# Performance work log

Measured on AMD Instinct MI355X. Metric: run time of the kernel, lower is better.

Reference implementation:

```python
import math
import jax, jax.numpy as jnp
import numpy as np

H = 1024
NH = 16
HD = H // NH
FF = 4096


def gelu_erf(x):
    return x * 0.5 * (1.0 + jax.lax.erf(x / jnp.sqrt(jnp.float32(2.0))))


def layernorm(x, gamma, beta, eps=1e-12):
    mean = x.mean(axis=-1, keepdims=True)
    var = ((x - mean) ** 2).mean(axis=-1, keepdims=True)
    return gamma * (x - mean) / jnp.sqrt(var + eps) + beta


def setup_inputs() -> dict:
    key = jax.random.key(0)
    ks = jax.random.split(key, 12)
    B, S = 2, 2048
    sc = 0.02
    return {
        "x": jax.random.normal(ks[0], (B, S, H), jnp.float32),
        "attention_mask": jnp.ones((B, S), jnp.int32),
        "Wq": jax.random.normal(ks[1], (H, H), jnp.float32) * sc,
        "bq": jnp.zeros((H,), jnp.float32),
        "Wk": jax.random.normal(ks[2], (H, H), jnp.float32) * sc,
        "bk": jnp.zeros((H,), jnp.float32),
        "Wv": jax.random.normal(ks[3], (H, H), jnp.float32) * sc,
        "bv": jnp.zeros((H,), jnp.float32),
        "Wo": jax.random.normal(ks[4], (H, H), jnp.float32) * sc,
        "bo": jnp.zeros((H,), jnp.float32),
        "ln1_g": jnp.ones((H,), jnp.float32),
        "ln1_b": jnp.zeros((H,), jnp.float32),
        "W1": jax.random.normal(ks[5], (H, FF), jnp.float32) * sc,
        "b1": jnp.zeros((FF,), jnp.float32),
        "W2": jax.random.normal(ks[6], (FF, H), jnp.float32) * sc,
        "b2": jnp.zeros((H,), jnp.float32),
        "ln2_g": jnp.ones((H,), jnp.float32),
        "ln2_b": jnp.zeros((H,), jnp.float32),
    }


def reference(x, attention_mask, Wq, bq, Wk, bk, Wv, bv, Wo, bo,
              ln1_g, ln1_b, W1, b1, W2, b2, ln2_g, ln2_b):
    B, S, _ = x.shape
    # QKV projections, split heads -> [B, NH, S, HD]
    def split(t):
        return t.reshape(B, S, NH, HD).transpose(0, 2, 1, 3)
    q = split(x @ Wq + bq)
    k = split(x @ Wk + bk)
    v = split(x @ Wv + bv)
    # scores [B, NH, S, S]
    s = jnp.einsum("bhqd,bhkd->bhqk", q, k) / math.sqrt(HD)
    mask = (attention_mask == 1)[:, None, None, :]  # [B,1,1,S]
    s = jnp.where(mask, s, -jnp.inf)
    p = jax.nn.softmax(s, axis=-1)
    a = jnp.einsum("bhqk,bhkd->bhqd", p, v)
    a = a.transpose(0, 2, 1, 3).reshape(B, S, H)  # merge heads
    a = a @ Wo + bo
    a = layernorm(a, ln1_g, ln1_b)  # NOTE: no residual in source
    m = gelu_erf(a @ W1 + b1) @ W2 + b2
    return layernorm(m, ln2_g, ln2_b)
```

## Files before the change

kernel.cpp:

```cpp
#include <hip/hip_runtime.h>
#include <hip/hip_bf16.h>
#include <math.h>

typedef __bf16 bf16;
typedef __attribute__((ext_vector_type(8))) __bf16 bf16x8;
typedef __attribute__((ext_vector_type(4))) __bf16 bf16x4;
typedef __attribute__((ext_vector_type(4))) float f32x4;
typedef __attribute__((ext_vector_type(4))) short short4v;

#define HDIM 1024
#define NHEAD 16
#define HD 64
#define FFDIM 4096
#define BATCH 2
#define SEQ 2048
#define M_TOK 4096
#define NSPLIT 2
#define PSTRIDE ((size_t)M_TOK * HDIM)

static __device__ __forceinline__ void async_load16(const bf16* g, bf16* l) {
  __builtin_amdgcn_global_load_lds(
      (const __attribute__((address_space(1))) void*)g,
      (__attribute__((address_space(3))) void*)l, 16, 0, 0);
}

static __device__ __forceinline__ f32x4 mfma16_bf16(bf16x4 a, bf16x4 b, f32x4 c) {
#if defined(__HIP_DEVICE_COMPILE__)
#if __has_builtin(__builtin_amdgcn_mfma_f32_16x16x16bf16_1k)
  return __builtin_amdgcn_mfma_f32_16x16x16bf16_1k(
      __builtin_bit_cast(short4v, a), __builtin_bit_cast(short4v, b), c, 0, 0, 0);
#else
  return __builtin_amdgcn_mfma_f32_16x16x16_bf16(a, b, c, 0, 0, 0);
#endif
#else
  return c;
#endif
}

__global__ __launch_bounds__(256)
void prep_kernel(const float* __restrict__ x,
                 const float* __restrict__ Wq, const float* __restrict__ Wk,
                 const float* __restrict__ Wv, const float* __restrict__ Wo,
                 const float* __restrict__ W1, const float* __restrict__ W2,
                 bf16* __restrict__ Xb, bf16* __restrict__ QKVT,
                 bf16* __restrict__ W1T, bf16* __restrict__ W2T)
{
  const int z = blockIdx.z;
  const int t = threadIdx.x;
  if (z == 12) {
    const size_t base = ((size_t)(blockIdx.y * 32 + blockIdx.x)) * 4096;
#pragma unroll
    for (int j = 0; j < 4; ++j) {
      const size_t i = base + j * 1024 + t * 4;
      f32x4 v = *(const f32x4*)(x + i);
      bf16x4 o;
#pragma unroll
      for (int k = 0; k < 4; ++k) o[k] = (bf16)v[k];
      *(bf16x4*)(Xb + i) = o;
    }
    return;
  }
  const float* ps; bf16* pd; int sld, dld;
  if (z < 4) {
    ps = (z == 0) ? Wq : (z == 1) ? Wk : (z == 2) ? Wv : Wo;
    pd = QKVT + (size_t)z * HDIM * HDIM; sld = 1024; dld = 1024;
  } else if (z < 8) {
    const int c = z - 4;
    ps = W1 + c * 1024; sld = 4096;
    pd = W1T + (size_t)c * 1024 * 1024; dld = 1024;
  } else {
    const int c = z - 8;
    ps = W2 + (size_t)c * 1024 * 1024; sld = 1024;
    pd = W2T + c * 1024; dld = 4096;
  }
  __shared__ float tile[32][33];
  const int tx = t & 31, ty = t >> 5;
  const int c0 = blockIdx.x * 32, r0 = blockIdx.y * 32;
#pragma unroll
  for (int i = 0; i < 32; i += 8)
    tile[ty + i][tx] = ps[(size_t)(r0 + ty + i) * sld + c0 + tx];
  __syncthreads();
#pragma unroll
  for (int i = 0; i < 32; i += 8)
    pd[(size_t)(c0 + ty + i) * dld + r0 + tx] = (bf16)tile[tx][ty + i];
}

template<int EPI>
__global__ __launch_bounds__(256)
void gemm_bt(const bf16* __restrict__ A, const bf16* __restrict__ Bt,
             const float* __restrict__ b0, const float* __restrict__ b1p,
             const float* __restrict__ b2p, void* __restrict__ Cout,
             int M, int N, int ldk, int kchunk)
{
  __shared__ __align__(16) bf16 As[128 * 64];
  __shared__ __align__(16) bf16 Bs[128 * 64];
  const int t = threadIdx.x;
  const int wave = t >> 6, lane = t & 63;
  const int lm = lane & 15, qd = lane >> 4;
  const int wm = (wave >> 1) * 64, wn = (wave & 1) * 64;
  const int bm = blockIdx.y * 128, bn = blockIdx.x * 128;
  const int kbeg = blockIdx.z * kchunk;

  f32x4 acc[4][4] = {};
  const int srow = t >> 3;
  const int schk = t & 7;

  for (int k0 = kbeg; k0 < kbeg + kchunk; k0 += 64) {
#pragma unroll
    for (int r = 0; r < 4; ++r) {
      const int row = r * 32 + srow;
      const int chunk = schk ^ (row & 7);
      async_load16(A + (size_t)(bm + row) * ldk + (k0 + chunk * 8),
                   (bf16*)((char*)As + r * 4096 + t * 16));
    }
#pragma unroll
    for (int r = 0; r < 4; ++r) {
      const int row = r * 32 + srow;
      const int chunk = schk ^ (row & 7);
      async_load16(Bt + (size_t)(bn + row) * ldk + (k0 + chunk * 8),
                   (bf16*)((char*)Bs + r * 4096 + t * 16));
    }
    __syncthreads();
#pragma unroll
    for (int ks = 0; ks < 2; ++ks) {
      bf16x8 av[4], bv[4];
#pragma unroll
      for (int mt = 0; mt < 4; ++mt) {
        const int row = wm + mt * 16 + lm;
        const int chunk = (ks * 4 + qd) ^ (row & 7);
        av[mt] = *(const bf16x8*)(As + row * 64 + chunk * 8);
      }
#pragma unroll
      for (int nt = 0; nt < 4; ++nt) {
        const int row = wn + nt * 16 + lm;
        const int chunk = (ks * 4 + qd) ^ (row & 7);
        bv[nt] = *(const bf16x8*)(Bs + row * 64 + chunk * 8);
      }
#pragma unroll
      for (int mt = 0; mt < 4; ++mt)
#pragma unroll
        for (int nt = 0; nt < 4; ++nt)
          acc[mt][nt] = __builtin_amdgcn_mfma_f32_16x16x32_bf16(bv[nt], av[mt], acc[mt][nt], 0, 0, 0);
    }
    __syncthreads();
  }

#pragma unroll
  for (int nt = 0; nt < 4; ++nt) {
    const int n0 = bn + wn + nt * 16 + qd * 4;
    f32x4 bsv = {0.f, 0.f, 0.f, 0.f};
    if (EPI == 2) bsv = *(const f32x4*)(b0 + n0);
    if (EPI == 3) {
      const int sect = n0 >> 10, c = n0 & 1023;
      const float* bp = (sect == 0) ? b0 : (sect == 1) ? b1p : b2p;
      bsv = *(const f32x4*)(bp + c);
    }
#pragma unroll
    for (int mt = 0; mt < 4; ++mt) {
      const int m = bm + wm + mt * 16 + lm;
      f32x4 v;
#pragma unroll
      for (int r = 0; r < 4; ++r) v[r] = acc[mt][nt][r] + bsv[r];
      if (EPI == 1) {
        *(f32x4*)((float*)Cout + (size_t)blockIdx.z * M * N + (size_t)m * N + n0) = v;
      } else if (EPI == 2) {
        bf16x4 o;
#pragma unroll
        for (int r = 0; r < 4; ++r) {
          const float z = v[r] * 0.70710678118f;
          const float az = fabsf(z);
          const float tt = __builtin_amdgcn_rcpf(fmaf(az, 0.3275911f, 1.0f));
          const float poly = tt * fmaf(tt, fmaf(tt, fmaf(tt, fmaf(tt, 1.061405429f,
                             -1.453152027f), 1.421413741f), -0.284496736f), 0.254829592f);
          const float e = __builtin_amdgcn_exp2f(az * az * -1.4426950408889634f);
          float erfv = 1.0f - poly * e;
          erfv = (z < 0.f) ? -erfv : erfv;
          o[r] = (bf16)(0.5f * v[r] * (1.0f + erfv));
        }
        *(bf16x4*)((bf16*)Cout + (size_t)m * N + n0) = o;
      } else {
        bf16* base = (bf16*)Cout;
        const int sect = n0 >> 10, c = n0 & 1023;
        if (sect < 2) {
          bf16x4 o;
#pragma unroll
          for (int r = 0; r < 4; ++r) o[r] = (bf16)v[r];
          *(bf16x4*)(base + (size_t)sect * M_TOK * HDIM + (size_t)m * HDIM + c) = o;
        } else {
          const int hh = c >> 6, dd = c & 63;
          const int bb = m >> 11, ss = m & 2047;
#pragma unroll
          for (int r = 0; r < 4; ++r)
            base[(size_t)2 * M_TOK * HDIM +
                 (size_t)((bb * NHEAD + hh) * HD + dd + r) * SEQ + ss] = (bf16)v[r];
        }
      }
    }
  }
}

__global__ __launch_bounds__(256)
void attn_kernel(const bf16* __restrict__ Q, const bf16* __restrict__ Kg,
                 const bf16* __restrict__ Vt, const int* __restrict__ mask,
                 float* __restrict__ Po, float* __restrict__ Lp)
{
  __shared__ __align__(16) bf16 Ks[64 * 64];
  __shared__ __align__(16) bf16 Vs[64 * 64];
  __shared__ float madd[64];

  const int t = threadIdx.x;
  const int wave = t >> 6, lane = t & 63;
  const int lm = lane & 15, qd = lane >> 4;
  const int bh = blockIdx.y;
  const int b = bh >> 4, h = bh & 15;
  const int q0 = blockIdx.x * 64;
  const int qg = q0 + wave * 16 + lm;
  const int split = blockIdx.z;
  const int kv_beg = split * (SEQ / NSPLIT);

  bf16x8 qf[2];
#pragma unroll
  for (int ks = 0; ks < 2; ++ks)
    qf[ks] = *(const bf16x8*)(Q + (size_t)(b * SEQ + qg) * HDIM + h * HD + ks * 32 + qd * 8);

  float l_lane = 0.f;
  f32x4 oacc[4] = {};

  const int srow = t >> 3, schk = t & 7;
  const float C = 0.1803368801f;

  for (int kv0 = kv_beg; kv0 < kv_beg + SEQ / NSPLIT; kv0 += 64) {
#pragma unroll
    for (int r = 0; r < 2; ++r) {
      const int row = r * 32 + srow;
      const int g = schk ^ (row & 7);
      async_load16(Kg + (size_t)(b * SEQ + kv0 + row) * HDIM + h * HD + g * 8,
                   (bf16*)((char*)Ks + r * 4096 + t * 16));
      async_load16(Vt + (size_t)(bh * HD + row) * SEQ + kv0 + g * 8,
                   (bf16*)((char*)Vs + r * 4096 + t * 16));
    }
    if (t < 64) madd[t] = (mask[b * SEQ + kv0 + t] == 1) ? 0.f : -1.0e30f;
    __syncthreads();

    f32x4 sacc[4] = {};
#pragma unroll
    for (int ks = 0; ks < 2; ++ks) {
#pragma unroll
      for (int nt = 0; nt < 4; ++nt) {
        const int row = nt * 16 + lm;
        const int c = (ks * 4 + qd) ^ (row & 7);
        bf16x8 kf = *(const bf16x8*)(Ks + row * 64 + c * 8);
        sacc[nt] = __builtin_amdgcn_mfma_f32_16x16x32_bf16(kf, qf[ks], sacc[nt], 0, 0, 0);
      }
    }

    bf16x4 pf4[4];
#pragma unroll
    for (int nt = 0; nt < 4; ++nt) {
      f32x4 ma = *(const f32x4*)(madd + nt * 16 + qd * 4);
#pragma unroll
      for (int r = 0; r < 4; ++r) {
        const float pv = __builtin_amdgcn_exp2f(fmaf(sacc[nt][r], C, ma[r]));
        l_lane += pv;
        pf4[nt][r] = (bf16)pv;
      }
    }

#pragma unroll
    for (int nt2 = 0; nt2 < 4; ++nt2) {
      const int row = nt2 * 16 + lm;
#pragma unroll
      for (int nt = 0; nt < 4; ++nt) {
        bf16x4 vf = *(const bf16x4*)(Vs + row * 64 +
                     (((nt * 2 + (qd >> 1)) ^ (row & 7)) * 8) + (qd & 1) * 4);
        oacc[nt2] = mfma16_bf16(vf, pf4[nt], oacc[nt2]);
      }
    }
    __syncthreads();
  }

  float l = l_lane;
  l += __shfl_xor(l, 16, 64);
  l += __shfl_xor(l, 32, 64);

  float* po = Po + ((size_t)(split * 32 + bh) * 64) * SEQ;
#pragma unroll
  for (int nt2 = 0; nt2 < 4; ++nt2)
#pragma unroll
    for (int r = 0; r < 4; ++r)
      po[(size_t)(nt2 * 16 + qd * 4 + r) * SEQ + q0 + wave * 16 + lm] = oacc[nt2][r];
  if (qd == 0)
    Lp[(size_t)(split * 32 + bh) * SEQ + q0 + wave * 16 + lm] = l;
}

__global__ __launch_bounds__(256)
void attn_merge(const float* __restrict__ Po, const float* __restrict__ Lp,
                bf16* __restrict__ Aout)
{
  const int t = threadIdx.x;
  const int bh = blockIdx.y;
  const int b = bh >> 4, h = bh & 15;
  const int s0 = blockIdx.x * 64;
  const int tok = t >> 2;
  const int dc = (t & 3) * 16;

  const float l = Lp[(size_t)bh * SEQ + s0 + tok] +
                  Lp[(size_t)(32 + bh) * SEQ + s0 + tok];
  const float inv = 1.0f / l;

  const float* p0 = Po + ((size_t)bh * 64) * SEQ + s0 + tok;
  const float* p1 = Po + ((size_t)(32 + bh) * 64) * SEQ + s0 + tok;
  bf16x8 o0, o1;
#pragma unroll
  for (int j = 0; j < 8; ++j)
    o0[j] = (bf16)((p0[(size_t)(dc + j) * SEQ] + p1[(size_t)(dc + j) * SEQ]) * inv);
#pragma unroll
  for (int j = 8; j < 16; ++j)
    o1[j - 8] = (bf16)((p0[(size_t)(dc + j) * SEQ] + p1[(size_t)(dc + j) * SEQ]) * inv);

  bf16* dst = Aout + (size_t)(b * SEQ + s0 + tok) * HDIM + h * HD + dc;
  *(bf16x8*)dst = o0;
  *(bf16x8*)(dst + 8) = o1;
}

template<int NP, int OUT_BF16>
__global__ __launch_bounds__(256)
void ln_sum(const float* __restrict__ p, const float* __restrict__ bias,
            const float* __restrict__ gamma, const float* __restrict__ beta,
            void* __restrict__ out)
{
  const int row = blockIdx.x;
  const int t = threadIdx.x;
  f32x4 v = *(const f32x4*)(p + (size_t)row * HDIM + t * 4);
#pragma unroll
  for (int np = 1; np < NP; ++np) {
    f32x4 u = *(const f32x4*)(p + np * PSTRIDE + (size_t)row * HDIM + t * 4);
#pragma unroll
    for (int j = 0; j < 4; ++j) v[j] += u[j];
  }
  f32x4 bv0 = *(const f32x4*)(bias + t * 4);
#pragma unroll
  for (int j = 0; j < 4; ++j) v[j] += bv0[j];

  float s = v[0] + v[1] + v[2] + v[3];
  float s2 = v[0] * v[0] + v[1] * v[1] + v[2] * v[2] + v[3] * v[3];
#pragma unroll
  for (int d = 1; d < 64; d <<= 1) { s += __shfl_xor(s, d, 64); s2 += __shfl_xor(s2, d, 64); }
  __shared__ float ss[4], ss2[4];
  const int wave = t >> 6, lane = t & 63;
  if (lane == 0) { ss[wave] = s; ss2[wave] = s2; }
  __syncthreads();
  s = ss[0] + ss[1] + ss[2] + ss[3];
  s2 = ss2[0] + ss2[1] + ss2[2] + ss2[3];
  const float mean = s * (1.0f / HDIM);
  const float var = s2 * (1.0f / HDIM) - mean * mean;
  const float rstd = rsqrtf(var + 1e-12f);
  f32x4 gv = *(const f32x4*)(gamma + t * 4);
  f32x4 bv = *(const f32x4*)(beta + t * 4);
  f32x4 y;
#pragma unroll
  for (int j = 0; j < 4; ++j) y[j] = gv[j] * (v[j] - mean) * rstd + bv[j];
  if (OUT_BF16) {
    bf16x4 o;
#pragma unroll
    for (int j = 0; j < 4; ++j) o[j] = (bf16)y[j];
    *(bf16x4*)((bf16*)out + (size_t)row * HDIM + t * 4) = o;
  } else {
    *(f32x4*)((float*)out + (size_t)row * HDIM + t * 4) = y;
  }
}

extern "C" void kernel_launch(void* const* d_in, const int* in_sizes, int n_in,
                              void* d_out, int out_size, void* d_ws, size_t ws_size,
                              hipStream_t stream)
{
  const float* x    = (const float*)d_in[0];
  const int*   am   = (const int*)d_in[1];
  const float* Wq   = (const float*)d_in[2];
  const float* bq   = (const float*)d_in[3];
  const float* Wk   = (const float*)d_in[4];
  const float* bk   = (const float*)d_in[5];
  const float* Wv   = (const float*)d_in[6];
  const float* bv   = (const float*)d_in[7];
  const float* Wo   = (const float*)d_in[8];
  const float* bo   = (const float*)d_in[9];
  const float* ln1g = (const float*)d_in[10];
  const float* ln1b = (const float*)d_in[11];
  const float* W1   = (const float*)d_in[12];
  const float* b1   = (const float*)d_in[13];
  const float* W2   = (const float*)d_in[14];
  const float* b2   = (const float*)d_in[15];
  const float* ln2g = (const float*)d_in[16];
  const float* ln2b = (const float*)d_in[17];

  char* ws = (char*)d_ws;
  const size_t MB = 1ull << 20;
  bf16*  W1T  = (bf16*)(ws + 0 * MB);
  bf16*  W2T  = (bf16*)(ws + 8 * MB);
  bf16*  Xb   = (bf16*)(ws + 16 * MB);
  bf16*  QKVT = (bf16*)(ws + 24 * MB);
  bf16*  WoT  = QKVT + (size_t)3 * HDIM * HDIM;
  bf16*  Qb   = (bf16*)(ws + 33 * MB);
  bf16*  Kb   = (bf16*)(ws + 41 * MB);
  bf16*  Vtb  = (bf16*)(ws + 49 * MB);
  float* Po   = (float*)(ws + 57 * MB);
  float* Lp   = (float*)(ws + 89 * MB);
  bf16*  Ab   = (bf16*)(ws + 16 * MB);
  float* Pw   = (float*)(ws + 33 * MB);
  bf16*  L1   = (bf16*)(ws + 65 * MB);
  bf16*  F1   = (bf16*)(ws + 16 * MB);
  float* Pf   = (float*)(ws + 48 * MB);

  prep_kernel<<<dim3(32, 32, 13), 256, 0, stream>>>(x, Wq, Wk, Wv, Wo, W1, W2,
                                                    Xb, QKVT, W1T, W2T);

  gemm_bt<3><<<dim3(3072 / 128, M_TOK / 128, 1), 256, 0, stream>>>(
      Xb, QKVT, bq, bk, bv, Qb, M_TOK, 3072, HDIM, HDIM);

  attn_kernel<<<dim3(SEQ / 64, BATCH * NHEAD, NSPLIT), 256, 0, stream>>>(
      Qb, Kb, Vtb, am, Po, Lp);
  attn_merge<<<dim3(SEQ / 64, BATCH * NHEAD), 256, 0, stream>>>(Po, Lp, Ab);

  gemm_bt<1><<<dim3(HDIM / 128, M_TOK / 128, 2), 256, 0, stream>>>(
      Ab, WoT, nullptr, nullptr, nullptr, Pw, M_TOK, HDIM, HDIM, 512);
  ln_sum<2, 1><<<M_TOK, 256, 0, stream>>>(Pw, bo, ln1g, ln1b, L1);

  gemm_bt<2><<<dim3(FFDIM / 128, M_TOK / 128, 1), 256, 0, stream>>>(
      L1, W1T, b1, nullptr, nullptr, F1, M_TOK, FFDIM, HDIM, HDIM);

  if (ws_size >= 113 * MB) {
    gemm_bt<1><<<dim3(HDIM / 128, M_TOK / 128, 4), 256, 0, stream>>>(
        F1, W2T, nullptr, nullptr, nullptr, Pf, M_TOK, HDIM, FFDIM, 1024);
    ln_sum<4, 0><<<M_TOK, 256, 0, stream>>>(Pf, b2, ln2g, ln2b, (float*)d_out);
  } else {
    gemm_bt<1><<<dim3(HDIM / 128, M_TOK / 128, 2), 256, 0, stream>>>(
        F1, W2T, nullptr, nullptr, nullptr, Pf, M_TOK, HDIM, FFDIM, 2048);
    ln_sum<2, 0><<<M_TOK, 256, 0, stream>>>(Pf, b2, ln2g, ln2b, (float*)d_out);
  }
}
```

Baseline: 388.0 us.

## Load K/V fragments directly from global via blocked V layout, drop LDS staging

The QKV GEMM epilogue now writes V in a blocked layout of 16-key chunks, so each lane can read its MFMA B-fragment as a contiguous bf16x4 straight from global memory. The attention kernel no longer stages K/V through shared memory and drops both __syncthreads per tile. Each wave now processes two 16-query tiles so every loaded K/V fragment is used twice, and the grid is halved. This removes LDS traffic and barriers but relies on L1/L2 for K/V reuse across the four waves, and it raises register pressure.

```diff
diff --git a/kernel.cpp b/kernel.cpp
--- a/kernel.cpp
+++ b/kernel.cpp
@@ -187,12 +187,14 @@
           for (int r = 0; r < 4; ++r) o[r] = (bf16)v[r];
           *(bf16x4*)(base + (size_t)sect * M_TOK * HDIM + (size_t)m * HDIM + c) = o;
         } else {
-          const int hh = c >> 6, dd = c & 63;
+          const int hh = c >> 6, d0 = c & 63;
           const int bb = m >> 11, ss = m & 2047;
+          const int kb = ss >> 4, j = ss & 15;
+          bf16* vb = base + (size_t)2 * M_TOK * HDIM +
+                     (size_t)(bb * NHEAD + hh) * (SEQ / 16) * HD * 16;
 #pragma unroll
           for (int r = 0; r < 4; ++r)
-            base[(size_t)2 * M_TOK * HDIM +
-                 (size_t)((bb * NHEAD + hh) * HD + dd + r) * SEQ + ss] = (bf16)v[r];
+            vb[((size_t)kb * HD + d0 + r) * 16 + j] = (bf16)v[r];
         }
       }
     }
@@ -201,96 +203,103 @@
 
 __global__ __launch_bounds__(256)
 void attn_kernel(const bf16* __restrict__ Q, const bf16* __restrict__ Kg,
-                 const bf16* __restrict__ Vt, const int* __restrict__ mask,
+                 const bf16* __restrict__ VB, const int* __restrict__ mask,
                  float* __restrict__ Po, float* __restrict__ Lp)
 {
-  __shared__ __align__(16) bf16 Ks[64 * 64];
-  __shared__ __align__(16) bf16 Vs[64 * 64];
-  __shared__ float madd[64];
-
   const int t = threadIdx.x;
   const int wave = t >> 6, lane = t & 63;
   const int lm = lane & 15, qd = lane >> 4;
   const int bh = blockIdx.y;
   const int b = bh >> 4, h = bh & 15;
-  const int q0 = blockIdx.x * 64;
-  const int qg = q0 + wave * 16 + lm;
+  const int q0 = blockIdx.x * 128 + wave * 32;
   const int split = blockIdx.z;
   const int kv_beg = split * (SEQ / NSPLIT);
 
-  bf16x8 qf[2];
-#pragma unroll
-  for (int ks = 0; ks < 2; ++ks)
-    qf[ks] = *(const bf16x8*)(Q + (size_t)(b * SEQ + qg) * HDIM + h * HD + ks * 32 + qd * 8);
-
-  float l_lane = 0.f;
-  f32x4 oacc[4] = {};
-
-  const int srow = t >> 3, schk = t & 7;
+  bf16x8 qf[2][2];
+#pragma unroll
+  for (int qt = 0; qt < 2; ++qt)
+#pragma unroll
+    for (int ks = 0; ks < 2; ++ks)
+      qf[qt][ks] = *(const bf16x8*)(Q + (size_t)(b * SEQ + q0 + qt * 16 + lm) * HDIM +
+                                    h * HD + ks * 32 + qd * 8);
+
+  const bf16* Kp = Kg + (size_t)(b * SEQ + kv_beg + lm) * HDIM + h * HD + qd * 8;
+  const bf16* Vp = VB + (size_t)bh * (SEQ / 16) * HD * 16 +
+                   (size_t)(kv_beg >> 4) * (HD * 16) + lm * 16 + qd * 4;
+  const int* Mp = mask + b * SEQ + kv_beg + qd * 4;
+
+  float l_lane[2] = {0.f, 0.f};
+  f32x4 oacc[2][4] = {};
   const float C = 0.1803368801f;
 
-  for (int kv0 = kv_beg; kv0 < kv_beg + SEQ / NSPLIT; kv0 += 64) {
-#pragma unroll
-    for (int r = 0; r < 2; ++r) {
-      const int row = r * 32 + srow;
-      const int g = schk ^ (row & 7);
-      async_load16(Kg + (size_t)(b * SEQ + kv0 + row) * HDIM + h * HD + g * 8,
-                   (bf16*)((char*)Ks + r * 4096 + t * 16));
-      async_load16(Vt + (size_t)(bh * HD + row) * SEQ + kv0 + g * 8,
-                   (bf16*)((char*)Vs + r * 4096 + t * 16));
-    }
-    if (t < 64) madd[t] = (mask[b * SEQ + kv0 + t] == 1) ? 0.f : -1.0e30f;
-    __syncthreads();
-
-    f32x4 sacc[4] = {};
-#pragma unroll
-    for (int ks = 0; ks < 2; ++ks) {
+  for (int it = 0; it < (SEQ / NSPLIT) / 64; ++it) {
+    bf16x8 kf[2][4];
+#pragma unroll
+    for (int nt = 0; nt < 4; ++nt)
+#pragma unroll
+      for (int ks = 0; ks < 2; ++ks)
+        kf[ks][nt] = *(const bf16x8*)(Kp + (size_t)nt * 16 * HDIM + ks * 32);
+
+    bf16x4 vf[4][4];
+#pragma unroll
+    for (int nt2 = 0; nt2 < 4; ++nt2)
+#pragma unroll
+      for (int nt = 0; nt < 4; ++nt)
+        vf[nt2][nt] = *(const bf16x4*)(Vp + nt * (16 * HD * 16 / 16) + nt2 * 256);
+
+    int4 mi[4];
+#pragma unroll
+    for (int nt = 0; nt < 4; ++nt) mi[nt] = *(const int4*)(Mp + nt * 16);
+
+    bf16x4 pf[2][4];
+#pragma unroll
+    for (int qt = 0; qt < 2; ++qt) {
+      f32x4 sacc[4] = {};
+#pragma unroll
+      for (int ks = 0; ks < 2; ++ks)
+#pragma unroll
+        for (int nt = 0; nt < 4; ++nt)
+          sacc[nt] = __builtin_amdgcn_mfma_f32_16x16x32_bf16(kf[ks][nt], qf[qt][ks], sacc[nt], 0, 0, 0);
 #pragma unroll
       for (int nt = 0; nt < 4; ++nt) {
-        const int row = nt * 16 + lm;
-        const int c = (ks * 4 + qd) ^ (row & 7);
-        bf16x8 kf = *(const bf16x8*)(Ks + row * 64 + c * 8);
-        sacc[nt] = __builtin_amdgcn_mfma_f32_16x16x32_bf16(kf, qf[ks], sacc[nt], 0, 0, 0);
+        const int* mv = (const int*)&mi[nt];
+#pragma unroll
+        for (int r = 0; r < 4; ++r) {
+          const float ma = (mv[r] == 1) ? 0.f : -1.0e30f;
+          const float pv = __builtin_amdgcn_exp2f(fmaf(sacc[nt][r], C, ma));
+          l_lane[qt] += pv;
+          pf[qt][nt][r] = (bf16)pv;
+        }
       }
     }
 
-    bf16x4 pf4[4];
-#pragma unroll
-    for (int nt = 0; nt < 4; ++nt) {
-      f32x4 ma = *(const f32x4*)(madd + nt * 16 + qd * 4);
-#pragma unroll
-      for (int r = 0; r < 4; ++r) {
-        const float pv = __builtin_amdgcn_exp2f(fmaf(sacc[nt][r], C, ma[r]));
-        l_lane += pv;
-        pf4[nt][r] = (bf16)pv;
-      }
-    }
-
-#pragma unroll
-    for (int nt2 = 0; nt2 < 4; ++nt2) {
-      const int row = nt2 * 16 + lm;
-#pragma unroll
-      for (int nt = 0; nt < 4; ++nt) {
-        bf16x4 vf = *(const bf16x4*)(Vs + row * 64 +
-                     (((nt * 2 + (qd >> 1)) ^ (row & 7)) * 8) + (qd & 1) * 4);
-        oacc[nt2] = mfma16_bf16(vf, pf4[nt], oacc[nt2]);
-      }
-    }
-    __syncthreads();
-  }
-
-  float l = l_lane;
-  l += __shfl_xor(l, 16, 64);
-  l += __shfl_xor(l, 32, 64);
-
-  float* po = Po + ((size_t)(split * 32 + bh) * 64) * SEQ;
-#pragma unroll
-  for (int nt2 = 0; nt2 < 4; ++nt2)
-#pragma unroll
-    for (int r = 0; r < 4; ++r)
-      po[(size_t)(nt2 * 16 + qd * 4 + r) * SEQ + q0 + wave * 16 + lm] = oacc[nt2][r];
-  if (qd == 0)
-    Lp[(size_t)(split * 32 + bh) * SEQ + q0 + wave * 16 + lm] = l;
+#pragma unroll
+    for (int nt2 = 0; nt2 < 4; ++nt2)
+#pragma unroll
+      for (int nt = 0; nt < 4; ++nt)
+#pragma unroll
+        for (int qt = 0; qt < 2; ++qt)
+          oacc[qt][nt2] = mfma16_bf16(vf[nt2][nt], pf[qt][nt], oacc[qt][nt2]);
+
+    Kp += (size_t)64 * HDIM;
+    Vp += 4 * (HD * 16);
+    Mp += 64;
+  }
+
+  float* po = Po + (size_t)(split * 32 + bh) * 64 * SEQ;
+#pragma unroll
+  for (int qt = 0; qt < 2; ++qt) {
+    float l = l_lane[qt];
+    l += __shfl_xor(l, 16, 64);
+    l += __shfl_xor(l, 32, 64);
+#pragma unroll
+    for (int nt2 = 0; nt2 < 4; ++nt2)
+#pragma unroll
+      for (int r = 0; r < 4; ++r)
+        po[(size_t)(nt2 * 16 + qd * 4 + r) * SEQ + q0 + qt * 16 + lm] = oacc[qt][nt2][r];
+    if (qd == 0)
+      Lp[(size_t)(split * 32 + bh) * SEQ + q0 + qt * 16 + lm] = l;
+  }
 }
 
 __global__ __launch_bounds__(256)
@@ -402,7 +411,7 @@
   bf16*  WoT  = QKVT + (size_t)3 * HDIM * HDIM;
   bf16*  Qb   = (bf16*)(ws + 33 * MB);
   bf16*  Kb   = (bf16*)(ws + 41 * MB);
-  bf16*  Vtb  = (bf16*)(ws + 49 * MB);
+  bf16*  VBb  = (bf16*)(ws + 49 * MB);
   float* Po   = (float*)(ws + 57 * MB);
   float* Lp   = (float*)(ws + 89 * MB);
   bf16*  Ab   = (bf16*)(ws + 16 * MB);
@@ -417,8 +426,8 @@
   gemm_bt<3><<<dim3(3072 / 128, M_TOK / 128, 1), 256, 0, stream>>>(
       Xb, QKVT, bq, bk, bv, Qb, M_TOK, 3072, HDIM, HDIM);
 
-  attn_kernel<<<dim3(SEQ / 64, BATCH * NHEAD, NSPLIT), 256, 0, stream>>>(
-      Qb, Kb, Vtb, am, Po, Lp);
+  attn_kernel<<<dim3(SEQ / 128, BATCH * NHEAD, NSPLIT), 256, 0, stream>>>(
+      Qb, Kb, VBb, am, Po, Lp);
   attn_merge<<<dim3(SEQ / 64, BATCH * NHEAD), 256, 0, stream>>>(Po, Lp, Ab);
 
   gemm_bt<1><<<dim3(HDIM / 128, M_TOK / 128, 2), 256, 0, stream>>>(
```

New measurement: 419.5 us. 1.08x slower.
